# Optimization experiments

Measured on AMD Instinct MI355X. Metric: run time of the kernel, lower is better.

The kernel has to match this reference:

```python
import jax, jax.numpy as jnp
import numpy as np

N_HEADS = 4
NUM_GROUPS = 32
EPS = 1e-6


def _nin(t, W, b):
    # 1x1 conv as dense over channel dim: [B,C,H,W] x [C,D] -> [B,D,H,W]
    return jnp.einsum('bchw,cd->bdhw', t, W) + b[None, :, None, None]


def setup_inputs() -> dict:
    key = jax.random.key(0)
    ks = jax.random.split(key, 12)
    B, C, H, W = 8, 256, 32, 32
    Tc = 512
    Cin = C + Tc  # 768
    x = jax.random.normal(ks[0], (B, C, H, W), dtype=jnp.float32)
    text_feat = jax.random.normal(ks[1], (B, Tc), dtype=jnp.float32)
    gn_gamma = jnp.ones((Cin,), dtype=jnp.float32)
    gn_beta = jnp.zeros((Cin,), dtype=jnp.float32)
    scale = 1.0 / np.sqrt(Cin)
    W0 = jax.random.normal(ks[2], (Cin, C), dtype=jnp.float32) * scale
    b0 = jnp.zeros((C,), dtype=jnp.float32)
    W1 = jax.random.normal(ks[3], (Cin, C), dtype=jnp.float32) * scale
    b1 = jnp.zeros((C,), dtype=jnp.float32)
    W2 = jax.random.normal(ks[4], (Cin, C), dtype=jnp.float32) * scale
    b2 = jnp.zeros((C,), dtype=jnp.float32)
    return {"x": x, "text_feat": text_feat, "gn_gamma": gn_gamma, "gn_beta": gn_beta,
            "W0": W0, "b0": b0, "W1": W1, "b1": b1, "W2": W2, "b2": b2}


def reference(x, text_feat, gn_gamma, gn_beta, W0, b0, W1, b1, W2, b2):
    B, C, H, W = x.shape
    # broadcast text features spatially and concat on channel dim
    tf = jnp.broadcast_to(text_feat[:, :, None, None], (B, text_feat.shape[1], H, W))
    h = jnp.concatenate([x, tf], axis=1)  # [B, C+Tc, H, W]
    Ctot = h.shape[1]
    # GroupNorm(32, Ctot), eps=1e-6
    hg = h.reshape(B, NUM_GROUPS, Ctot // NUM_GROUPS, H, W)
    mu = hg.mean(axis=(2, 3, 4), keepdims=True)
    var = hg.var(axis=(2, 3, 4), keepdims=True)
    hn = ((hg - mu) * jax.lax.rsqrt(var + EPS)).reshape(B, Ctot, H, W)
    hn = hn * gn_gamma[None, :, None, None] + gn_beta[None, :, None, None]
    q = _nin(hn, W0, b0)
    k = _nin(hn, W1, b1)
    v = _nin(hn, W2, b2)
    Ch = C // N_HEADS
    qh = q.reshape(B * N_HEADS, Ch, H, W)
    kh = k.reshape(B * N_HEADS, Ch, H, W)
    vh = v.reshape(B * N_HEADS, Ch, H, W)
    # full HW x HW attention scores, softmax over flattened key positions
    w = jnp.einsum('bchw,bcij->bhwij', qh, kh) * (Ch ** -0.5)
    w = jax.nn.softmax(w.reshape(B * N_HEADS, H, W, H * W), axis=-1)
    w = w.reshape(B * N_HEADS, H, W, H, W)
    ho = jnp.einsum('bhwij,bcij->bchw', w, vh).reshape(B, C, H, W)
    return x + ho
```

## Files before the change

### kernel.cpp

```cpp
#include <hip/hip_runtime.h>
#include <math.h>

#define BATCH 8
#define CX 256
#define TC 512
#define CIN 768
#define HW_TOT 1024
#define NH 4
#define CHD 64

typedef __attribute__((ext_vector_type(8))) short short8;
typedef __attribute__((ext_vector_type(4))) short s4v;
typedef __attribute__((ext_vector_type(4))) float floatx4;

static __device__ __forceinline__ short f2bf(float f) {
    union { float f; unsigned u; } c; c.f = f;
    unsigned r = (c.u + 0x7fffu + ((c.u >> 16) & 1u)) >> 16;
    return (short)r;
}

__global__ __launch_bounds__(256)
void gn_kernel(const float* __restrict__ x, const float* __restrict__ tf,
               const float* __restrict__ gamma, const float* __restrict__ beta,
               float* __restrict__ scale, float* __restrict__ shift) {
    const int b = blockIdx.x >> 5;
    const int g = blockIdx.x & 31;
    const int t = threadIdx.x;
    const int w = t >> 6, lane = t & 63;

    float s = 0.f, ss = 0.f;
    #pragma unroll
    for (int rr = 0; rr < 6; rr++) {
        const int row = w * 6 + rr;
        const int cg = g * 24 + row;
        if (cg < CX) {
            const float4* p = (const float4*)(x + ((size_t)b * CX + cg) * HW_TOT);
            #pragma unroll
            for (int i = 0; i < 4; i++) {
                float4 v = p[lane + 64 * i];
                s += v.x + v.y + v.z + v.w;
                ss += v.x * v.x + v.y * v.y + v.z * v.z + v.w * v.w;
            }
        } else {
            float v = tf[b * TC + cg - CX];
            s += 16.f * v;
            ss += 16.f * v * v;
        }
    }
    #pragma unroll
    for (int d = 1; d < 64; d <<= 1) {
        s += __shfl_xor(s, d);
        ss += __shfl_xor(ss, d);
    }
    __shared__ float rs_[4], rss_[4];
    if (lane == 0) { rs_[w] = s; rss_[w] = ss; }
    __syncthreads();
    const float S  = rs_[0] + rs_[1] + rs_[2] + rs_[3];
    const float SS = rss_[0] + rss_[1] + rss_[2] + rss_[3];
    const float inv_n = 1.f / (24 * 1024);
    const float mean = S * inv_n;
    const float var = SS * inv_n - mean * mean;
    const float r = rsqrtf(var + 1e-6f);
    if (t < 24) {
        int cg = g * 24 + t;
        float sc = gamma[cg] * r;
        scale[b * CIN + cg] = sc;
        shift[b * CIN + cg] = beta[cg] - mean * sc;
    }
}

__global__ __launch_bounds__(256)
void prep_kernel(const float* __restrict__ x, const float* __restrict__ tf,
                 const float* __restrict__ scale, const float* __restrict__ shift,
                 const float* __restrict__ W0, const float* __restrict__ W1,
                 const float* __restrict__ W2,
                 short* __restrict__ hnT, short* __restrict__ Wt,
                 float* __restrict__ tc) {
    __shared__ float hs[TC];
    __shared__ float red[4][64];
    const int bx = blockIdx.x;
    const int t = threadIdx.x;
    if (bx < 256) {
        int id = (bx & 31) * 256 + t;
        int b = id >> 10;
        const float* xb = x + (size_t)b * CX * HW_TOT + (id & 1023);
        const float* scb = scale + b * CIN;
        const float* shb = shift + b * CIN;
        short* outp = hnT + (size_t)id * CX;
        int c0base = (bx >> 5) * 32;
        for (int c0 = c0base; c0 < c0base + 32; c0 += 8) {
            short8 o;
            #pragma unroll
            for (int i = 0; i < 8; i++) {
                float v = xb[(size_t)(c0 + i) * HW_TOT];
                o[i] = f2bf(v * scb[c0 + i] + shb[c0 + i]);
            }
            *(short8*)(outp + c0) = o;
        }
    } else if (bx < 268) {
        int m = bx - 256;
        int dg = (m % 3) * 256 + t;
        int which = dg >> 8, d = dg & 255;
        const float* Wm = (which == 0) ? W0 : (which == 1) ? W1 : W2;
        int c0base = (m / 3) * 64;
        for (int c0 = c0base; c0 < c0base + 64; c0 += 8) {
            short8 o;
            #pragma unroll
            for (int i = 0; i < 8; i++) o[i] = f2bf(Wm[(size_t)(c0 + i) * CX + d]);
            *(short8*)(Wt + (size_t)dg * CX + c0) = o;
        }
    } else {
        int m = bx - 268;
        int b = m & 7, dt = m >> 3;
        int which = dt >> 2, d0 = (dt & 3) * 64;
        const float* Wm = (which == 0) ? W0 : (which == 1) ? W1 : W2;
        for (int c = t; c < TC; c += 256)
            hs[c] = tf[b * TC + c] * scale[b * CIN + CX + c] + shift[b * CIN + CX + c];
        __syncthreads();
        int td = t & 63, tq = t >> 6;
        float acc = 0.f;
        const float* wp = Wm + (size_t)(CX + tq * 128) * CX + d0 + td;
        for (int c = 0; c < 128; c++)
            acc = fmaf(hs[tq * 128 + c], wp[(size_t)c * CX], acc);
        red[tq][td] = acc;
        __syncthreads();
        if (t < 64)
            tc[b * CIN + which * CX + d0 + t] = red[0][t] + red[1][t] + red[2][t] + red[3][t];
    }
}

__global__ __launch_bounds__(256)
void qkv_gemm(const short* __restrict__ hnT, const short* __restrict__ Wt,
              const float* __restrict__ tc,
              const float* __restrict__ b0, const float* __restrict__ b1,
              const float* __restrict__ b2,
              short* __restrict__ qb, short* __restrict__ kb, short* __restrict__ vb) {
    const int hw0 = blockIdx.x * 128, dt = blockIdx.y, b = blockIdx.z;
    const int dg0 = dt * 128;
    const int which = dt >> 1;
    const bool OV = (which == 2);

    __shared__ short At[128 * 40];
    __shared__ short Bt[128 * 40];

    const int t = threadIdx.x;
    const int w = t >> 6, l = t & 63;
    const int wm = w >> 1, wn = w & 1;
    const int l15 = l & 15, q = l >> 4;

    const int srow = t >> 1, sch = (t & 1) * 16;
    const short* gA = hnT + (size_t)(b * HW_TOT + hw0 + srow) * CX + sch;
    const short* gB = Wt + (size_t)(dg0 + srow) * CX + sch;
    short* lA = At + srow * 40 + sch;
    short* lB = Bt + srow * 40 + sch;

    floatx4 acc[4][4] = {};
    for (int k0 = 0; k0 < CX; k0 += 32) {
        __syncthreads();
        *(short8*)lA       = *(const short8*)(gA + k0);
        *(short8*)(lA + 8) = *(const short8*)(gA + k0 + 8);
        *(short8*)lB       = *(const short8*)(gB + k0);
        *(short8*)(lB + 8) = *(const short8*)(gB + k0 + 8);
        __syncthreads();
        const short* aBase = OV ? Bt : At;
        const short* bBase = OV ? At : Bt;
        short8 af[4], bf[4];
        #pragma unroll
        for (int mt = 0; mt < 4; mt++)
            af[mt] = *(const short8*)(aBase + (wm * 64 + mt * 16 + l15) * 40 + q * 8);
        #pragma unroll
        for (int nt = 0; nt < 4; nt++)
            bf[nt] = *(const short8*)(bBase + (wn * 64 + nt * 16 + l15) * 40 + q * 8);
        #pragma unroll
        for (int mt = 0; mt < 4; mt++)
            #pragma unroll
            for (int nt = 0; nt < 4; nt++)
                acc[mt][nt] = __builtin_amdgcn_mfma_f32_16x16x32_bf16(
                    af[mt], bf[nt], acc[mt][nt], 0, 0, 0);
    }

    __syncthreads();
    const float* bias = (which == 0) ? b0 : (which == 1) ? b1 : b2;
    short* epi = At + w * (16 * 72);

    float colAdd[4];
    if (!OV) {
        #pragma unroll
        for (int nt = 0; nt < 4; nt++) {
            int cl = (dt & 1) * 128 + wn * 64 + l15 + nt * 16;
            colAdd[nt] = bias[cl] + tc[b * CIN + which * CX + cl];
        }
    }
    const int row_l = l >> 2, ch = l & 3;
    #pragma unroll
    for (int mt = 0; mt < 4; mt++) {
        #pragma unroll
        for (int rr = 0; rr < 4; rr++) {
            float radd = 0.f;
            if (OV) {
                int rl = (dt & 1) * 128 + wm * 64 + mt * 16 + q * 4 + rr;
                radd = bias[rl] + tc[b * CIN + 2 * CX + rl];
            }
            #pragma unroll
            for (int nt = 0; nt < 4; nt++) {
                float val = acc[mt][nt][rr] + (OV ? radd : colAdd[nt]);
                epi[(q * 4 + rr) * 72 + l15 + nt * 16] = f2bf(val);
            }
        }
        short8 v0 = *(const short8*)(epi + row_l * 72 + ch * 16);
        short8 v1 = *(const short8*)(epi + row_l * 72 + ch * 16 + 8);
        if (!OV) {
            short* outp = (which == 0) ? qb : kb;
            size_t off = (size_t)(b * HW_TOT + hw0 + wm * 64 + mt * 16 + row_l) * CX
                       + (dt & 1) * 128 + wn * 64 + ch * 16;
            *(short8*)(outp + off) = v0;
            *(short8*)(outp + off + 8) = v1;
        } else {
            size_t off = (size_t)(b * CX + (dt & 1) * 128 + wm * 64 + mt * 16 + row_l) * HW_TOT
                       + hw0 + wn * 64 + ch * 16;
            *(short8*)(vb + off) = v0;
            *(short8*)(vb + off + 8) = v1;
        }
    }
}

__global__ __launch_bounds__(256)
void attn_part(const short* __restrict__ qb, const short* __restrict__ kb,
               const short* __restrict__ vb,
               float* __restrict__ opart, float* __restrict__ lpart) {
    const int qt = blockIdx.x, bh = blockIdx.y, sp = blockIdx.z;
    const int b = bh >> 2, h = bh & 3;
    const int hw0 = qt * 64;

    __shared__ short Qs[64 * 72];
    __shared__ short Ks[64 * 72];
    __shared__ short Vs[64 * 72];

    const int t = threadIdx.x;
    const int w = t >> 6, l = t & 63;
    const int l15 = l & 15, q = l >> 4;
    const int srow = t >> 2, sch = (t & 3) * 16;

    {
        const short* gq = qb + (size_t)(b * HW_TOT + hw0 + srow) * CX + h * CHD + sch;
        *(short8*)(Qs + srow * 72 + sch)     = *(const short8*)gq;
        *(short8*)(Qs + srow * 72 + sch + 8) = *(const short8*)(gq + 8);
    }

    short8 pk0, pk1, pv0, pv1;
    {
        const int j0 = sp * 512;
        const short* gk = kb + (size_t)(b * HW_TOT + j0 + srow) * CX + h * CHD + sch;
        pk0 = *(const short8*)gk;
        pk1 = *(const short8*)(gk + 8);
        const short* gv = vb + (size_t)(b * CX + h * CHD + srow) * HW_TOT + j0 + sch;
        pv0 = *(const short8*)gv;
        pv1 = *(const short8*)(gv + 8);
    }
    __syncthreads();
    const short8 aq0 = *(const short8*)(Qs + (w * 16 + l15) * 72 + q * 8);
    const short8 aq1 = *(const short8*)(Qs + (w * 16 + l15) * 72 + 32 + q * 8);

    floatx4 oacc[4] = {};
    float lsum = 0.f;

    for (int jj = 0; jj < 8; jj++) {
        *(short8*)(Ks + srow * 72 + sch)     = pk0;
        *(short8*)(Ks + srow * 72 + sch + 8) = pk1;
        *(short8*)(Vs + srow * 72 + sch)     = pv0;
        *(short8*)(Vs + srow * 72 + sch + 8) = pv1;
        __syncthreads();

        if (jj < 7) {
            const int j0 = sp * 512 + (jj + 1) * 64;
            const short* gk = kb + (size_t)(b * HW_TOT + j0 + srow) * CX + h * CHD + sch;
            pk0 = *(const short8*)gk;
            pk1 = *(const short8*)(gk + 8);
            const short* gv = vb + (size_t)(b * CX + h * CHD + srow) * HW_TOT + j0 + sch;
            pv0 = *(const short8*)gv;
            pv1 = *(const short8*)(gv + 8);
        }

        floatx4 sacc[4] = {};
        #pragma unroll
        for (int nt = 0; nt < 4; nt++) {
            short8 kf0 = *(const short8*)(Ks + (nt * 16 + l15) * 72 + q * 8);
            short8 kf1 = *(const short8*)(Ks + (nt * 16 + l15) * 72 + 32 + q * 8);
            sacc[nt] = __builtin_amdgcn_mfma_f32_16x16x32_bf16(kf0, aq0, sacc[nt], 0, 0, 0);
            sacc[nt] = __builtin_amdgcn_mfma_f32_16x16x32_bf16(kf1, aq1, sacc[nt], 0, 0, 0);
        }

        short8 pf[2];
        #pragma unroll
        for (int nt = 0; nt < 4; nt++)
            #pragma unroll
            for (int r = 0; r < 4; r++) {
                float e = __expf(fmaf(sacc[nt][r], 0.125f, -10.f));
                lsum += e;
                pf[nt >> 1][(nt & 1) * 4 + r] = f2bf(e);
            }

        #pragma unroll
        for (int ct = 0; ct < 4; ct++) {
            const short* vr = Vs + (ct * 16 + l15) * 72;
            #pragma unroll
            for (int kcc = 0; kcc < 2; kcc++) {
                s4v vlo = *(const s4v*)(vr + kcc * 32 + q * 4);
                s4v vhi = *(const s4v*)(vr + kcc * 32 + 16 + q * 4);
                short8 vf = __builtin_shufflevector(vlo, vhi, 0, 1, 2, 3, 4, 5, 6, 7);
                oacc[ct] = __builtin_amdgcn_mfma_f32_16x16x32_bf16(vf, pf[kcc], oacc[ct], 0, 0, 0);
            }
        }
        __syncthreads();
    }

    float* op = opart + ((size_t)(sp * BATCH + b) * CX) * HW_TOT;
    #pragma unroll
    for (int ct = 0; ct < 4; ct++)
        #pragma unroll
        for (int r = 0; r < 4; r++) {
            int c = h * CHD + ct * 16 + q * 4 + r;
            op[(size_t)c * HW_TOT + hw0 + w * 16 + l15] = oacc[ct][r];
        }
    lsum += __shfl_xor(lsum, 16);
    lsum += __shfl_xor(lsum, 32);
    if (q == 0)
        lpart[(size_t)(sp * 32 + bh) * HW_TOT + hw0 + w * 16 + l15] = lsum;
}

__global__ __launch_bounds__(256)
void attn_epi(const float* __restrict__ opart, const float* __restrict__ lpart,
              const float* __restrict__ x, float* __restrict__ out) {
    const int idx = (blockIdx.x * 256 + threadIdx.x) * 4;
    const int b = idx >> 18, c = (idx >> 10) & 255, hw = idx & 1023;
    const int bh = b * 4 + (c >> 6);
    const size_t lo = (size_t)bh * HW_TOT + hw;
    float4 l0 = *(const float4*)(lpart + lo);
    float4 l1 = *(const float4*)(lpart + 32 * HW_TOT + lo);
    float4 o0 = *(const float4*)(opart + idx);
    float4 o1 = *(const float4*)(opart + BATCH * CX * HW_TOT + idx);
    float4 xv = *(const float4*)(x + idx);
    float4 ov;
    ov.x = xv.x + (o0.x + o1.x) / (l0.x + l1.x);
    ov.y = xv.y + (o0.y + o1.y) / (l0.y + l1.y);
    ov.z = xv.z + (o0.z + o1.z) / (l0.z + l1.z);
    ov.w = xv.w + (o0.w + o1.w) / (l0.w + l1.w);
    *(float4*)(out + idx) = ov;
}

extern "C" void kernel_launch(void* const* d_in, const int* in_sizes, int n_in,
                              void* d_out, int out_size, void* d_ws, size_t ws_size,
                              hipStream_t stream) {
    (void)in_sizes; (void)n_in; (void)out_size; (void)ws_size;
    const float* x     = (const float*)d_in[0];
    const float* tf    = (const float*)d_in[1];
    const float* gamma = (const float*)d_in[2];
    const float* beta  = (const float*)d_in[3];
    const float* W0 = (const float*)d_in[4];
    const float* b0 = (const float*)d_in[5];
    const float* W1 = (const float*)d_in[6];
    const float* b1 = (const float*)d_in[7];
    const float* W2 = (const float*)d_in[8];
    const float* b2 = (const float*)d_in[9];

    char* ws = (char*)d_ws;
    float* scale  = (float*)(ws);
    float* shift  = (float*)(ws + 24576);
    float* tcb    = (float*)(ws + 49152);
    short* Wt     = (short*)(ws + 73728);
    short* hnT    = (short*)(ws + 466944);
    short* qb     = (short*)(ws + 4661248);
    short* kb     = (short*)(ws + 8855552);
    short* vb     = (short*)(ws + 13049856);
    float* opart  = (float*)(ws + 17244160);
    float* lpart  = (float*)(ws + 34021376);

    hipLaunchKernelGGL(gn_kernel, dim3(256), dim3(256), 0, stream,
                       x, tf, gamma, beta, scale, shift);
    hipLaunchKernelGGL(prep_kernel, dim3(364), dim3(256), 0, stream,
                       x, tf, scale, shift, W0, W1, W2, hnT, Wt, tcb);
    hipLaunchKernelGGL(qkv_gemm, dim3(8, 6, BATCH), dim3(256), 0, stream,
                       hnT, Wt, tcb, b0, b1, b2, qb, kb, vb);
    hipLaunchKernelGGL(attn_part, dim3(16, 32, 2), dim3(256), 0, stream,
                       qb, kb, vb, opart, lpart);
    hipLaunchKernelGGL(attn_epi, dim3(2048), dim3(256), 0, stream,
                       opart, lpart, x, (float*)d_out);
}
```

Baseline: 128.3 us.

## Raise parallelism: split-K text projection, smaller QKV tiles, 4-way attention split

```diff
diff --git a/kernel.cpp b/kernel.cpp
--- a/kernel.cpp
+++ b/kernel.cpp
@@ -8,6 +8,7 @@
 #define HW_TOT 1024
 #define NH 4
 #define CHD 64
+#define SPLIT 4
 
 typedef __attribute__((ext_vector_type(8))) short short8;
 typedef __attribute__((ext_vector_type(4))) short s4v;
@@ -22,11 +23,13 @@
 __global__ __launch_bounds__(256)
 void gn_kernel(const float* __restrict__ x, const float* __restrict__ tf,
                const float* __restrict__ gamma, const float* __restrict__ beta,
-               float* __restrict__ scale, float* __restrict__ shift) {
+               float* __restrict__ scale, float* __restrict__ shift,
+               float* __restrict__ tc) {
     const int b = blockIdx.x >> 5;
     const int g = blockIdx.x & 31;
     const int t = threadIdx.x;
     const int w = t >> 6, lane = t & 63;
+    if (blockIdx.x < 24) tc[blockIdx.x * 256 + t] = 0.f;
 
     float s = 0.f, ss = 0.f;
     #pragma unroll
@@ -76,7 +79,7 @@
                  const float* __restrict__ W2,
                  short* __restrict__ hnT, short* __restrict__ Wt,
                  float* __restrict__ tc) {
-    __shared__ float hs[TC];
+    __shared__ float hs[128];
     __shared__ float red[4][64];
     const int bx = blockIdx.x;
     const int t = threadIdx.x;
@@ -111,21 +114,26 @@
         }
     } else {
         int m = bx - 268;
-        int b = m & 7, dt = m >> 3;
+        int ks = m & 3;
+        int b = (m >> 2) & 7, dt = m >> 5;
         int which = dt >> 2, d0 = (dt & 3) * 64;
         const float* Wm = (which == 0) ? W0 : (which == 1) ? W1 : W2;
-        for (int c = t; c < TC; c += 256)
-            hs[c] = tf[b * TC + c] * scale[b * CIN + CX + c] + shift[b * CIN + CX + c];
+        if (t < 128) {
+            int c = ks * 128 + t;
+            hs[t] = tf[b * TC + c] * scale[b * CIN + CX + c] + shift[b * CIN + CX + c];
+        }
         __syncthreads();
         int td = t & 63, tq = t >> 6;
         float acc = 0.f;
-        const float* wp = Wm + (size_t)(CX + tq * 128) * CX + d0 + td;
-        for (int c = 0; c < 128; c++)
-            acc = fmaf(hs[tq * 128 + c], wp[(size_t)c * CX], acc);
+        const float* wp = Wm + (size_t)(CX + ks * 128 + tq * 32) * CX + d0 + td;
+        #pragma unroll 8
+        for (int c = 0; c < 32; c++)
+            acc = fmaf(hs[tq * 32 + c], wp[(size_t)c * CX], acc);
         red[tq][td] = acc;
         __syncthreads();
         if (t < 64)
-            tc[b * CIN + which * CX + d0 + t] = red[0][t] + red[1][t] + red[2][t] + red[3][t];
+            atomicAdd(&tc[b * CIN + which * CX + d0 + t],
+                      red[0][t] + red[1][t] + red[2][t] + red[3][t]);
     }
 }
 
@@ -135,92 +143,94 @@
               const float* __restrict__ b0, const float* __restrict__ b1,
               const float* __restrict__ b2,
               short* __restrict__ qb, short* __restrict__ kb, short* __restrict__ vb) {
-    const int hw0 = blockIdx.x * 128, dt = blockIdx.y, b = blockIdx.z;
-    const int dg0 = dt * 128;
-    const int which = dt >> 1;
+    const int hw0 = blockIdx.x * 64, dt = blockIdx.y, b = blockIdx.z;
+    const int which = dt >> 2;
+    const int col0 = (dt & 3) * 64;
+    const int dg0 = which * 256 + col0;
     const bool OV = (which == 2);
 
-    __shared__ short At[128 * 40];
-    __shared__ short Bt[128 * 40];
+    __shared__ short At[64 * 72];
+    __shared__ short Bt[64 * 72];
 
     const int t = threadIdx.x;
     const int w = t >> 6, l = t & 63;
     const int wm = w >> 1, wn = w & 1;
     const int l15 = l & 15, q = l >> 4;
-
-    const int srow = t >> 1, sch = (t & 1) * 16;
+    const int srow = t >> 2, sch = (t & 3) * 16;
+
     const short* gA = hnT + (size_t)(b * HW_TOT + hw0 + srow) * CX + sch;
     const short* gB = Wt + (size_t)(dg0 + srow) * CX + sch;
-    short* lA = At + srow * 40 + sch;
-    short* lB = Bt + srow * 40 + sch;
-
-    floatx4 acc[4][4] = {};
-    for (int k0 = 0; k0 < CX; k0 += 32) {
-        __syncthreads();
-        *(short8*)lA       = *(const short8*)(gA + k0);
-        *(short8*)(lA + 8) = *(const short8*)(gA + k0 + 8);
-        *(short8*)lB       = *(const short8*)(gB + k0);
-        *(short8*)(lB + 8) = *(const short8*)(gB + k0 + 8);
-        __syncthreads();
-        const short* aBase = OV ? Bt : At;
-        const short* bBase = OV ? At : Bt;
-        short8 af[4], bf[4];
-        #pragma unroll
-        for (int mt = 0; mt < 4; mt++)
-            af[mt] = *(const short8*)(aBase + (wm * 64 + mt * 16 + l15) * 40 + q * 8);
-        #pragma unroll
-        for (int nt = 0; nt < 4; nt++)
-            bf[nt] = *(const short8*)(bBase + (wn * 64 + nt * 16 + l15) * 40 + q * 8);
-        #pragma unroll
-        for (int mt = 0; mt < 4; mt++)
-            #pragma unroll
-            for (int nt = 0; nt < 4; nt++)
-                acc[mt][nt] = __builtin_amdgcn_mfma_f32_16x16x32_bf16(
-                    af[mt], bf[nt], acc[mt][nt], 0, 0, 0);
+
+    floatx4 acc[2][2] = {};
+    for (int k0 = 0; k0 < CX; k0 += 64) {
+        __syncthreads();
+        *(short8*)(At + srow * 72 + sch)     = *(const short8*)(gA + k0);
+        *(short8*)(At + srow * 72 + sch + 8) = *(const short8*)(gA + k0 + 8);
+        *(short8*)(Bt + srow * 72 + sch)     = *(const short8*)(gB + k0);
+        *(short8*)(Bt + srow * 72 + sch + 8) = *(const short8*)(gB + k0 + 8);
+        __syncthreads();
+        const short* aB = OV ? Bt : At;
+        const short* bB = OV ? At : Bt;
+        #pragma unroll
+        for (int kc = 0; kc < 2; kc++) {
+            short8 af[2], bf2[2];
+            #pragma unroll
+            for (int mt = 0; mt < 2; mt++)
+                af[mt] = *(const short8*)(aB + (wm * 32 + mt * 16 + l15) * 72 + kc * 32 + q * 8);
+            #pragma unroll
+            for (int nt = 0; nt < 2; nt++)
+                bf2[nt] = *(const short8*)(bB + (wn * 32 + nt * 16 + l15) * 72 + kc * 32 + q * 8);
+            #pragma unroll
+            for (int mt = 0; mt < 2; mt++)
+                #pragma unroll
+                for (int nt = 0; nt < 2; nt++)
+                    acc[mt][nt] = __builtin_amdgcn_mfma_f32_16x16x32_bf16(
+                        af[mt], bf2[nt], acc[mt][nt], 0, 0, 0);
+        }
     }
 
     __syncthreads();
     const float* bias = (which == 0) ? b0 : (which == 1) ? b1 : b2;
-    short* epi = At + w * (16 * 72);
-
-    float colAdd[4];
     if (!OV) {
-        #pragma unroll
-        for (int nt = 0; nt < 4; nt++) {
-            int cl = (dt & 1) * 128 + wn * 64 + l15 + nt * 16;
-            colAdd[nt] = bias[cl] + tc[b * CIN + which * CX + cl];
-        }
-    }
-    const int row_l = l >> 2, ch = l & 3;
-    #pragma unroll
-    for (int mt = 0; mt < 4; mt++) {
-        #pragma unroll
-        for (int rr = 0; rr < 4; rr++) {
-            float radd = 0.f;
-            if (OV) {
-                int rl = (dt & 1) * 128 + wm * 64 + mt * 16 + q * 4 + rr;
-                radd = bias[rl] + tc[b * CIN + 2 * CX + rl];
+        float cadd[2];
+        #pragma unroll
+        for (int nt = 0; nt < 2; nt++) {
+            int d = col0 + wn * 32 + nt * 16 + l15;
+            cadd[nt] = bias[d] + tc[b * CIN + which * CX + d];
+        }
+        #pragma unroll
+        for (int mt = 0; mt < 2; mt++)
+            #pragma unroll
+            for (int rr = 0; rr < 4; rr++)
+                #pragma unroll
+                for (int nt = 0; nt < 2; nt++)
+                    At[(wm * 32 + mt * 16 + q * 4 + rr) * 72 + wn * 32 + nt * 16 + l15]
+                        = f2bf(acc[mt][nt][rr] + cadd[nt]);
+    } else {
+        #pragma unroll
+        for (int mt = 0; mt < 2; mt++)
+            #pragma unroll
+            for (int rr = 0; rr < 4; rr++) {
+                int d = col0 + wm * 32 + mt * 16 + q * 4 + rr;
+                float radd = bias[d] + tc[b * CIN + 2 * CX + d];
+                #pragma unroll
+                for (int nt = 0; nt < 2; nt++)
+                    At[(wm * 32 + mt * 16 + q * 4 + rr) * 72 + wn * 32 + nt * 16 + l15]
+                        = f2bf(acc[mt][nt][rr] + radd);
             }
-            #pragma unroll
-            for (int nt = 0; nt < 4; nt++) {
-                float val = acc[mt][nt][rr] + (OV ? radd : colAdd[nt]);
-                epi[(q * 4 + rr) * 72 + l15 + nt * 16] = f2bf(val);
-            }
-        }
-        short8 v0 = *(const short8*)(epi + row_l * 72 + ch * 16);
-        short8 v1 = *(const short8*)(epi + row_l * 72 + ch * 16 + 8);
-        if (!OV) {
-            short* outp = (which == 0) ? qb : kb;
-            size_t off = (size_t)(b * HW_TOT + hw0 + wm * 64 + mt * 16 + row_l) * CX
-                       + (dt & 1) * 128 + wn * 64 + ch * 16;
-            *(short8*)(outp + off) = v0;
-            *(short8*)(outp + off + 8) = v1;
-        } else {
-            size_t off = (size_t)(b * CX + (dt & 1) * 128 + wm * 64 + mt * 16 + row_l) * HW_TOT
-                       + hw0 + wn * 64 + ch * 16;
-            *(short8*)(vb + off) = v0;
-            *(short8*)(vb + off + 8) = v1;
-        }
+    }
+    __syncthreads();
+    short8 v0 = *(const short8*)(At + srow * 72 + sch);
+    short8 v1 = *(const short8*)(At + srow * 72 + sch + 8);
+    if (!OV) {
+        short* outp = (which == 0) ? qb : kb;
+        size_t off = (size_t)(b * HW_TOT + hw0 + srow) * CX + col0 + sch;
+        *(short8*)(outp + off) = v0;
+        *(short8*)(outp + off + 8) = v1;
+    } else {
+        size_t off = (size_t)(b * CX + col0 + srow) * HW_TOT + hw0 + sch;
+        *(short8*)(vb + off) = v0;
+        *(short8*)(vb + off + 8) = v1;
     }
 }
 
@@ -249,7 +259,7 @@
 
     short8 pk0, pk1, pv0, pv1;
     {
-        const int j0 = sp * 512;
+        const int j0 = sp * (HW_TOT / SPLIT);
         const short* gk = kb + (size_t)(b * HW_TOT + j0 + srow) * CX + h * CHD + sch;
         pk0 = *(const short8*)gk;
         pk1 = *(const short8*)(gk + 8);
@@ -264,15 +274,15 @@
     floatx4 oacc[4] = {};
     float lsum = 0.f;
 
-    for (int jj = 0; jj < 8; jj++) {
+    for (int jj = 0; jj < HW_TOT / SPLIT / 64; jj++) {
         *(short8*)(Ks + srow * 72 + sch)     = pk0;
         *(short8*)(Ks + srow * 72 + sch + 8) = pk1;
         *(short8*)(Vs + srow * 72 + sch)     = pv0;
         *(short8*)(Vs + srow * 72 + sch + 8) = pv1;
         __syncthreads();
 
-        if (jj < 7) {
-            const int j0 = sp * 512 + (jj + 1) * 64;
+        if (jj < HW_TOT / SPLIT / 64 - 1) {
+            const int j0 = sp * (HW_TOT / SPLIT) + (jj + 1) * 64;
             const short* gk = kb + (size_t)(b * HW_TOT + j0 + srow) * CX + h * CHD + sch;
             pk0 = *(const short8*)gk;
             pk1 = *(const short8*)(gk + 8);
@@ -335,16 +345,21 @@
     const int b = idx >> 18, c = (idx >> 10) & 255, hw = idx & 1023;
     const int bh = b * 4 + (c >> 6);
     const size_t lo = (size_t)bh * HW_TOT + hw;
-    float4 l0 = *(const float4*)(lpart + lo);
-    float4 l1 = *(const float4*)(lpart + 32 * HW_TOT + lo);
-    float4 o0 = *(const float4*)(opart + idx);
-    float4 o1 = *(const float4*)(opart + BATCH * CX * HW_TOT + idx);
+    float4 osum = make_float4(0.f, 0.f, 0.f, 0.f);
+    float4 lsum = make_float4(0.f, 0.f, 0.f, 0.f);
+    #pragma unroll
+    for (int s = 0; s < SPLIT; s++) {
+        float4 o = *(const float4*)(opart + (size_t)s * BATCH * CX * HW_TOT + idx);
+        float4 lv = *(const float4*)(lpart + (size_t)s * 32 * HW_TOT + lo);
+        osum.x += o.x; osum.y += o.y; osum.z += o.z; osum.w += o.w;
+        lsum.x += lv.x; lsum.y += lv.y; lsum.z += lv.z; lsum.w += lv.w;
+    }
     float4 xv = *(const float4*)(x + idx);
     float4 ov;
-    ov.x = xv.x + (o0.x + o1.x) / (l0.x + l1.x);
-    ov.y = xv.y + (o0.y + o1.y) / (l0.y + l1.y);
-    ov.z = xv.z + (o0.z + o1.z) / (l0.z + l1.z);
-    ov.w = xv.w + (o0.w + o1.w) / (l0.w + l1.w);
+    ov.x = xv.x + osum.x / lsum.x;
+    ov.y = xv.y + osum.y / lsum.y;
+    ov.z = xv.z + osum.z / lsum.z;
+    ov.w = xv.w + osum.w / lsum.w;
     *(float4*)(out + idx) = ov;
 }
 
@@ -373,15 +388,15 @@
     short* kb     = (short*)(ws + 8855552);
     short* vb     = (short*)(ws + 13049856);
     float* opart  = (float*)(ws + 17244160);
-    float* lpart  = (float*)(ws + 34021376);
+    float* lpart  = (float*)(ws + 50798592);
 
     hipLaunchKernelGGL(gn_kernel, dim3(256), dim3(256), 0, stream,
-                       x, tf, gamma, beta, scale, shift);
-    hipLaunchKernelGGL(prep_kernel, dim3(364), dim3(256), 0, stream,
+                       x, tf, gamma, beta, scale, shift, tcb);
+    hipLaunchKernelGGL(prep_kernel, dim3(652), dim3(256), 0, stream,
                        x, tf, scale, shift, W0, W1, W2, hnT, Wt, tcb);
-    hipLaunchKernelGGL(qkv_gemm, dim3(8, 6, BATCH), dim3(256), 0, stream,
+    hipLaunchKernelGGL(qkv_gemm, dim3(16, 12, BATCH), dim3(256), 0, stream,
                        hnT, Wt, tcb, b0, b1, b2, qb, kb, vb);
-    hipLaunchKernelGGL(attn_part, dim3(16, 32, 2), dim3(256), 0, stream,
+    hipLaunchKernelGGL(attn_part, dim3(16, 32, SPLIT), dim3(256), 0, stream,
                        qb, kb, vb, opart, lpart);
     hipLaunchKernelGGL(attn_epi, dim3(2048), dim3(256), 0, stream,
                        opart, lpart, x, (float*)d_out);
```

New measurement: 129.4 us. No clear change (+0.9%).
